# Kernel optimization log

Measured on AMD Instinct MI355X. Metric: run time of the kernel, lower is better.

The kernel has to match this reference:

```python
import jax, jax.numpy as jnp
import numpy as np

B, S, H = 2, 2048, 1024
N_HEADS = 16
HEAD_DIM = H // N_HEADS


def setup_inputs() -> dict:
    key = jax.random.key(0)
    ks = jax.random.split(key, 7)
    scale = 0.02
    return {
        "q": jax.random.normal(ks[0], (B, S, H), dtype=jnp.float32),
        "k": jax.random.normal(ks[1], (B, S, H), dtype=jnp.float32),
        "v": jax.random.normal(ks[2], (B, S, H), dtype=jnp.float32),
        "Wq": jax.random.normal(ks[3], (H, H), dtype=jnp.float32) * scale,
        "Wk": jax.random.normal(ks[4], (H, H), dtype=jnp.float32) * scale,
        "Wv": jax.random.normal(ks[5], (H, H), dtype=jnp.float32) * scale,
        "Wo": jax.random.normal(ks[6], (H, H), dtype=jnp.float32) * scale,
    }


def reference(q, k, v, Wq, Wk, Wv, Wo):
    b, i, _ = q.shape
    _, j, _ = k.shape
    # torch.nn.Linear(bias=False): y = x @ W.T
    qp = q @ Wq.T
    kp = k @ Wk.T
    vp = v @ Wv.T
    # NOTE: original uses .view(b, n_heads, i, head_dim) with NO transpose,
    # i.e. a raw reshape of the (b, i, hidden) layout. Replicate exactly.
    qh = qp.reshape(b, N_HEADS, i, HEAD_DIM)
    kh = kp.reshape(b, N_HEADS, j, HEAD_DIM)
    vh = vp.reshape(b, N_HEADS, j, HEAD_DIM)
    attn_score = jnp.einsum("bnid,bnjd->bnij", qh, kh) / (HEAD_DIM ** 0.5)
    attn_weight = jax.nn.softmax(attn_score, axis=3)
    x = jnp.einsum("bnij,bnjd->bnid", attn_weight, vh)  # [b, n, i, d]
    # rearrange 'b n i d -> b i (n d)'
    x = jnp.transpose(x, (0, 2, 1, 3)).reshape(b, i, H)
    out = x @ Wo.T
    return (out, attn_weight)
```

## Files before the change

### kernel.cpp

```cpp
#include <hip/hip_runtime.h>
#include <hip/hip_bf16.h>

#define DEVI __device__ __forceinline__

constexpr int kS  = 2048;
constexpr int kH  = 1024;
constexpr int kD  = 64;
constexpr int kBS = 4096;
constexpr int kHeadEls = kS * kD;

typedef __attribute__((ext_vector_type(4))) float f32x4;
typedef __attribute__((ext_vector_type(8))) __bf16 bf16x8;
typedef __attribute__((ext_vector_type(8))) unsigned short u16x8;
typedef __attribute__((ext_vector_type(2))) unsigned int u32x2;

DEVI unsigned short f2bf(float f) {
  unsigned int u = __builtin_bit_cast(unsigned int, f);
  u = u + 0x7FFFu + ((u >> 16) & 1u);
  return (unsigned short)(u >> 16);
}
DEVI float fast_exp2(float x) { float r; asm("v_exp_f32 %0, %1" : "=v"(r) : "v"(x)); return r; }
DEVI unsigned int cvt_pk(float lo, float hi) {
  unsigned int r; asm("v_cvt_pk_bf16_f32 %0, %1, %2" : "=v"(r) : "v"(lo), "v"(hi)); return r;
}
DEVI bf16x8 cvt8(const f32x4 a, const f32x4 b) {
  union { unsigned int u[4]; bf16x8 v; } r;
  r.u[0] = cvt_pk(a[0], a[1]); r.u[1] = cvt_pk(a[2], a[3]);
  r.u[2] = cvt_pk(b[0], b[1]); r.u[3] = cvt_pk(b[2], b[3]);
  return r.v;
}
DEVI float bf2f(unsigned int lo16) {
  return __builtin_bit_cast(float, lo16 << 16);
}

#define GLDS16(g, l) __builtin_amdgcn_global_load_lds( \
    (const __attribute__((address_space(1))) void*)(g), \
    (__attribute__((address_space(3))) void*)(l), 16, 0, 0)

__global__ __launch_bounds__(256) void cvt_w(
    const float* __restrict__ s0, const float* __restrict__ s1, const float* __restrict__ s2,
    unsigned short* __restrict__ d0, unsigned short* __restrict__ d1, unsigned short* __restrict__ d2)
{
  const int m = blockIdx.y;
  const float* s = m == 0 ? s0 : m == 1 ? s1 : s2;
  unsigned short* d = m == 0 ? d0 : m == 1 ? d1 : d2;
  const int i = (blockIdx.x * 256 + threadIdx.x) * 8;
  f32x4 a = *(const f32x4*)(s + i);
  f32x4 b = *(const f32x4*)(s + i + 4);
  union { unsigned int u[4]; u16x8 v; } r;
  r.u[0] = cvt_pk(a[0], a[1]); r.u[1] = cvt_pk(a[2], a[3]);
  r.u[2] = cvt_pk(b[0], b[1]); r.u[3] = cvt_pk(b[2], b[3]);
  *(u16x8*)(d + i) = r.v;
}

template<bool PROJ>
__global__ __launch_bounds__(256, 3) void gemm_k(
    const void* __restrict__ Aq, const void* __restrict__ Ak, const void* __restrict__ Av,
    const void* __restrict__ Bq, const void* __restrict__ Bk, const void* __restrict__ Bv,
    void* __restrict__ Cq, void* __restrict__ Ck, void* __restrict__ Cv)
{
  constexpr int K = kH;
  __shared__ __align__(16) unsigned char As[2][PROJ ? 16384 : 8192];
  __shared__ __align__(16) unsigned char Bs[2][PROJ ? 8192 : 16384];

  const int z = PROJ ? blockIdx.z : 0;
  const void* Ap = z == 0 ? Aq : z == 1 ? Ak : Av;
  const void* Bp = z == 0 ? Bq : z == 1 ? Bk : Bv;
  void*       Cp = z == 0 ? Cq : z == 1 ? Ck : Cv;

  const int tid  = threadIdx.x;
  const int lane = tid & 63, wv = tid >> 6;
  const int l15  = lane & 15, lg = lane >> 4;
  const int m0 = blockIdx.y * 128, n0 = blockIdx.x * 128;
  const int wM = (wv & 1) * 64, wN = (wv >> 1) * 64;

  const char* aSrc[PROJ ? 4 : 2];
  if constexpr (PROJ) {
#pragma unroll
    for (int c = 0; c < 4; ++c) {
      const int row = c * 32 + wv * 8 + (lane >> 3);
      const int cb  = ((lane & 7) * 16) ^ ((row & 7) << 4);
      aSrc[c] = (const char*)Ap + ((size_t)(m0 + row) * K) * 4 + cb;
    }
  } else {
#pragma unroll
    for (int c = 0; c < 2; ++c) {
      const int row = c * 64 + (tid >> 2);
      const int cb  = ((tid & 3) * 16) ^ (((row >> 1) & 3) << 4);
      aSrc[c] = (const char*)Ap + ((size_t)(m0 + row) * K) * 2 + cb;
    }
  }
  const char* bSrc[PROJ ? 2 : 4];
  if constexpr (PROJ) {
#pragma unroll
    for (int c = 0; c < 2; ++c) {
      const int row = c * 64 + (tid >> 2);
      const int cb  = ((tid & 3) * 16) ^ (((row >> 1) & 3) << 4);
      bSrc[c] = (const char*)Bp + ((size_t)(n0 + row) * K) * 2 + cb;
    }
  } else {
#pragma unroll
    for (int c = 0; c < 4; ++c) {
      const int row = c * 32 + wv * 8 + (lane >> 3);
      const int cb  = ((lane & 7) * 16) ^ ((row & 7) << 4);
      bSrc[c] = (const char*)Bp + ((size_t)(n0 + row) * K) * 4 + cb;
    }
  }

  int aoff[4], boff[4];
#pragma unroll
  for (int t = 0; t < 4; ++t) {
    const int rA = wM + t * 16 + l15;
    aoff[t] = PROJ ? (rA * 128 + ((lg * 32) ^ ((rA & 7) << 4)))
                   : (rA * 64  + ((lg * 16) ^ (((rA >> 1) & 3) << 4)));
    const int rB = wN + t * 16 + l15;
    boff[t] = PROJ ? (rB * 64  + ((lg * 16) ^ (((rB >> 1) & 3) << 4)))
                   : (rB * 128 + ((lg * 32) ^ ((rB & 7) << 4)));
  }

  f32x4 acc[4][4];
#pragma unroll
  for (int i = 0; i < 4; ++i)
#pragma unroll
    for (int j = 0; j < 4; ++j) acc[i][j] = {0.f, 0.f, 0.f, 0.f};

  auto STG = [&](int kk, int bb) {
    if constexpr (PROJ) {
#pragma unroll
      for (int c = 0; c < 4; ++c)
        GLDS16(aSrc[c] + (size_t)kk * 4, &As[bb][c * 4096 + wv * 1024]);
#pragma unroll
      for (int c = 0; c < 2; ++c)
        GLDS16(bSrc[c] + (size_t)kk * 2, &Bs[bb][c * 4096 + wv * 1024]);
    } else {
#pragma unroll
      for (int c = 0; c < 2; ++c)
        GLDS16(aSrc[c] + (size_t)kk * 2, &As[bb][c * 4096 + wv * 1024]);
#pragma unroll
      for (int c = 0; c < 4; ++c)
        GLDS16(bSrc[c] + (size_t)kk * 4, &Bs[bb][c * 4096 + wv * 1024]);
    }
  };

  STG(0, 0);
  __syncthreads();
  int cur = 0;
  for (int t = 0; t < K / 32; ++t) {
    if (t < K / 32 - 1) STG((t + 1) * 32, cur ^ 1);
    bf16x8 af[4], bfr[4];
#pragma unroll
    for (int x = 0; x < 4; ++x) {
      if constexpr (PROJ) {
        f32x4 p0 = *(const f32x4*)&As[cur][aoff[x]];
        f32x4 p1 = *(const f32x4*)&As[cur][aoff[x] ^ 16];
        af[x] = cvt8(p0, p1);
        bfr[x] = *(const bf16x8*)&Bs[cur][boff[x]];
      } else {
        af[x] = *(const bf16x8*)&As[cur][aoff[x]];
        f32x4 q0 = *(const f32x4*)&Bs[cur][boff[x]];
        f32x4 q1 = *(const f32x4*)&Bs[cur][boff[x] ^ 16];
        bfr[x] = cvt8(q0, q1);
      }
    }
#pragma unroll
    for (int mt = 0; mt < 4; ++mt)
#pragma unroll
      for (int nt = 0; nt < 4; ++nt)
        acc[mt][nt] = __builtin_amdgcn_mfma_f32_16x16x32_bf16(af[mt], bfr[nt], acc[mt][nt], 0, 0, 0);
    __syncthreads();
    cur ^= 1;
  }

  if constexpr (PROJ) {
    const bool vmode = (z == 2);
#pragma unroll
    for (int mt = 0; mt < 4; ++mt)
#pragma unroll
      for (int nt = 0; nt < 4; ++nt)
#pragma unroll
        for (int r = 0; r < 4; ++r) {
          const int row = m0 + wM + mt * 16 + lg * 4 + r;
          const int col = n0 + wN + nt * 16 + l15;
          const unsigned short hv = f2bf(acc[mt][nt][r]);
          if (!vmode) {
            ((unsigned short*)Cp)[(size_t)row * kH + col] = hv;
          } else {
            const int bn = row >> 7;
            const int j  = ((row & 127) << 4) | (col >> 6);
            const int d  = col & 63;
            ((unsigned short*)Cp)[(size_t)bn * kHeadEls + (size_t)d * kS + j] = hv;
          }
        }
  } else {
#pragma unroll
    for (int mt = 0; mt < 4; ++mt)
#pragma unroll
      for (int nt = 0; nt < 4; ++nt)
#pragma unroll
        for (int r = 0; r < 4; ++r) {
          const int row = m0 + wM + mt * 16 + lg * 4 + r;
          const int col = n0 + wN + nt * 16 + l15;
          __builtin_nontemporal_store(acc[mt][nt][r], (float*)Cp + (size_t)row * kH + col);
        }
  }
}

__global__ __launch_bounds__(128, 2) void attn_rs(
    const unsigned short* __restrict__ QP,
    const unsigned short* __restrict__ KP,
    float* __restrict__ rsout)
{
  __shared__ __align__(16) unsigned short Kb[2][4096];

  const int tid  = threadIdx.x;
  const int lane = tid & 63, wv = tid >> 6;
  const int l15  = lane & 15, lg = lane >> 4;
  const int f = blockIdx.x;
  const int x = f & 7, r8 = f >> 3;
  const int bn = (r8 >> 5) * 8 + x;
  const int i0 = (r8 & 31) * 64;

  const char* Khb = (const char*)(KP + (size_t)bn * kHeadEls);
  const unsigned short* Qh = QP + (size_t)bn * kHeadEls;

  const int srw = tid >> 3, scl = (tid & 7) * 16;
  const int kbase = srw * 128 + (scl ^ ((srw & 7) << 4));

  auto STAGE = [&](int j0, int bb) {
#pragma unroll
    for (int p = 0; p < 4; ++p)
      GLDS16(Khb + (size_t)j0 * 128 + kbase + p * 2048, (char*)Kb[bb] + p * 2048 + tid * 16);
  };

  int koff[4][2];
#pragma unroll
  for (int ct = 0; ct < 4; ++ct) {
    const int rK = ct * 16 + l15;
#pragma unroll
    for (int h = 0; h < 2; ++h)
      koff[ct][h] = rK * 128 + ((h * 64 + lg * 16) ^ ((rK & 7) << 4));
  }

  bf16x8 qf[2][2];
#pragma unroll
  for (int m = 0; m < 2; ++m) {
    const int qr = i0 + wv * 32 + m * 16 + l15;
#pragma unroll
    for (int h = 0; h < 2; ++h)
      qf[m][h] = *(const bf16x8*)(Qh + (size_t)qr * kD + h * 32 + lg * 8);
  }
  const float cexp = 0.18033688011112042f;

  float rs[2] = {0.f, 0.f};
  STAGE(0, 0);
  __syncthreads();
  int cur = 0;
  for (int t = 0; t < 32; ++t) {
    if (t < 31) STAGE((t + 1) * 64, cur ^ 1);
#pragma unroll
    for (int ct = 0; ct < 4; ++ct) {
      const bf16x8 kb0 = *(const bf16x8*)((const char*)Kb[cur] + koff[ct][0]);
      const bf16x8 kb1 = *(const bf16x8*)((const char*)Kb[cur] + koff[ct][1]);
#pragma unroll
      for (int m = 0; m < 2; ++m) {
        f32x4 s = {0.f, 0.f, 0.f, 0.f};
        s = __builtin_amdgcn_mfma_f32_16x16x32_bf16(kb0, qf[m][0], s, 0, 0, 0);
        s = __builtin_amdgcn_mfma_f32_16x16x32_bf16(kb1, qf[m][1], s, 0, 0, 0);
        const float w0 = fast_exp2(s[0] * cexp), w1 = fast_exp2(s[1] * cexp);
        const float w2 = fast_exp2(s[2] * cexp), w3 = fast_exp2(s[3] * cexp);
        rs[m] += (w0 + w1) + (w2 + w3);
      }
    }
    __syncthreads();
    cur ^= 1;
  }
#pragma unroll
  for (int m = 0; m < 2; ++m) {
    rs[m] += __shfl_xor(rs[m], 16, 64);
    rs[m] += __shfl_xor(rs[m], 32, 64);
  }
  if (lg == 0) {
#pragma unroll
    for (int m = 0; m < 2; ++m)
      rsout[(size_t)bn * kS + i0 + wv * 32 + m * 16 + l15] = rs[m];
  }
}

__global__ __launch_bounds__(128, 2) void attn_main(
    const unsigned short* __restrict__ QP,
    const unsigned short* __restrict__ KP,
    const unsigned short* __restrict__ VPT,
    const float* __restrict__ rsb,
    float* __restrict__ AW,
    unsigned short* __restrict__ XB)
{
  __shared__ __align__(16) unsigned short Kb[2][4096];
  __shared__ __align__(16) unsigned short Vb[2][4096];
  __shared__ __align__(16) unsigned short Ws[4096];

  const int tid  = threadIdx.x;
  const int lane = tid & 63, wv = tid >> 6;
  const int l15  = lane & 15, lg = lane >> 4;
  const int f = blockIdx.x;
  const int x = f & 7, r8 = f >> 3;
  const int bn = (r8 >> 5) * 8 + x;
  const int i0 = (r8 & 31) * 64;
  const int b = bn >> 4, n = bn & 15;

  const char* Khb = (const char*)(KP + (size_t)bn * kHeadEls);
  const char* Vhb = (const char*)(VPT + (size_t)bn * kHeadEls);
  const unsigned short* Qh = QP + (size_t)bn * kHeadEls;

  const int srw = tid >> 3, scl = (tid & 7) * 16;
  const int sswz = scl ^ ((srw & 7) << 4);
  const int kbase = srw * 128 + sswz;
  const int vbase = srw * 4096 + sswz;

  auto STAGE_KV = [&](int j0, int bb) {
#pragma unroll
    for (int p = 0; p < 4; ++p) {
      GLDS16(Khb + (size_t)j0 * 128 + kbase + p * 2048,
             (char*)Kb[bb] + p * 2048 + tid * 16);
      GLDS16(Vhb + (size_t)j0 * 2 + vbase + (size_t)p * 65536,
             (char*)Vb[bb] + p * 2048 + tid * 16);
    }
  };

  int koff[4][2], voff[2][4], wswr[2][4], wsrd[2][2];
#pragma unroll
  for (int ct = 0; ct < 4; ++ct) {
    const int rK = ct * 16 + l15;
#pragma unroll
    for (int h = 0; h < 2; ++h)
      koff[ct][h] = rK * 128 + ((h * 64 + lg * 16) ^ ((rK & 7) << 4));
  }
#pragma unroll
  for (int jc = 0; jc < 2; ++jc)
#pragma unroll
    for (int dt = 0; dt < 4; ++dt) {
      const int d = dt * 16 + l15;
      voff[jc][dt] = d * 128 + ((jc * 64 + lg * 16) ^ ((d & 7) << 4));
    }
#pragma unroll
  for (int m = 0; m < 2; ++m) {
    const int rw = wv * 32 + m * 16 + l15;
#pragma unroll
    for (int ct = 0; ct < 4; ++ct)
      wswr[m][ct] = rw * 128 + ((ct * 32 + lg * 8) ^ ((rw & 7) << 4));
#pragma unroll
    for (int jc = 0; jc < 2; ++jc)
      wsrd[m][jc] = rw * 128 + ((jc * 64 + lg * 16) ^ ((rw & 7) << 4));
  }

  int awrd[8];
  float* awp[8];
#pragma unroll
  for (int u = 0; u < 8; ++u) {
    const int rw = wv * 32 + u * 4 + lg;
    awrd[u] = rw * 128 + ((l15 * 8) ^ ((rw & 7) << 4));
    awp[u]  = AW + ((size_t)bn * kS + i0 + rw) * kS + l15 * 4;
  }

  bf16x8 qf[2][2];
  float inv[2];
#pragma unroll
  for (int m = 0; m < 2; ++m) {
    const int qr = i0 + wv * 32 + m * 16 + l15;
#pragma unroll
    for (int h = 0; h < 2; ++h)
      qf[m][h] = *(const bf16x8*)(Qh + (size_t)qr * kD + h * 32 + lg * 8);
    inv[m] = 1.0f / rsb[(size_t)bn * kS + qr];
  }
  const float cexp = 0.18033688011112042f;

  f32x4 pv[2][4];
#pragma unroll
  for (int m = 0; m < 2; ++m)
#pragma unroll
    for (int dt = 0; dt < 4; ++dt) pv[m][dt] = {0.f, 0.f, 0.f, 0.f};

  STAGE_KV(0, 0);
  asm volatile("s_waitcnt vmcnt(0) lgkmcnt(0)" ::: "memory");
  __builtin_amdgcn_sched_barrier(0);
  __builtin_amdgcn_s_barrier();

  int cur = 0;
  for (int t = 0; t < 32; ++t) {
    if (t < 31) STAGE_KV((t + 1) * 64, cur ^ 1);
    __builtin_amdgcn_sched_barrier(0);
#pragma unroll
    for (int ct = 0; ct < 4; ++ct) {
      const bf16x8 kb0 = *(const bf16x8*)((const char*)Kb[cur] + koff[ct][0]);
      const bf16x8 kb1 = *(const bf16x8*)((const char*)Kb[cur] + koff[ct][1]);
#pragma unroll
      for (int m = 0; m < 2; ++m) {
        f32x4 s = {0.f, 0.f, 0.f, 0.f};
        s = __builtin_amdgcn_mfma_f32_16x16x32_bf16(kb0, qf[m][0], s, 0, 0, 0);
        s = __builtin_amdgcn_mfma_f32_16x16x32_bf16(kb1, qf[m][1], s, 0, 0, 0);
        f32x4 w;
#pragma unroll
        for (int r = 0; r < 4; ++r) w[r] = fast_exp2(s[r] * cexp) * inv[m];
        u32x2 pk; pk[0] = cvt_pk(w[0], w[1]); pk[1] = cvt_pk(w[2], w[3]);
        *(u32x2*)((char*)Ws + wswr[m][ct]) = pk;
      }
    }
#pragma unroll
    for (int jc = 0; jc < 2; ++jc) {
      const bf16x8 pa0 = *(const bf16x8*)((const char*)Ws + wsrd[0][jc]);
      const bf16x8 pa1 = *(const bf16x8*)((const char*)Ws + wsrd[1][jc]);
#pragma unroll
      for (int dt = 0; dt < 4; ++dt) {
        const bf16x8 vf = *(const bf16x8*)((const char*)Vb[cur] + voff[jc][dt]);
        pv[0][dt] = __builtin_amdgcn_mfma_f32_16x16x32_bf16(pa0, vf, pv[0][dt], 0, 0, 0);
        pv[1][dt] = __builtin_amdgcn_mfma_f32_16x16x32_bf16(pa1, vf, pv[1][dt], 0, 0, 0);
      }
    }
#pragma unroll
    for (int u = 0; u < 8; ++u) {
      const u32x2 pk = *(const u32x2*)((const char*)Ws + awrd[u]);
      f32x4 w;
      w[0] = bf2f(pk[0] & 0xFFFFu);
      w[1] = bf2f(pk[0] >> 16);
      w[2] = bf2f(pk[1] & 0xFFFFu);
      w[3] = bf2f(pk[1] >> 16);
      __builtin_nontemporal_store(w, (f32x4*)(awp[u] + t * 64));
    }
    if (t < 31) {
      asm volatile("s_waitcnt vmcnt(8) lgkmcnt(0)" ::: "memory");
      __builtin_amdgcn_sched_barrier(0);
      __builtin_amdgcn_s_barrier();
    }
    cur ^= 1;
  }

#pragma unroll
  for (int m = 0; m < 2; ++m)
#pragma unroll
    for (int dt = 0; dt < 4; ++dt)
#pragma unroll
      for (int r = 0; r < 4; ++r) {
        const int row = b * kS + i0 + wv * 32 + m * 16 + lg * 4 + r;
        const int col = n * 64 + dt * 16 + l15;
        XB[(size_t)row * kH + col] = f2bf(pv[m][dt][r]);
      }
}

extern "C" void kernel_launch(void* const* d_in, const int* in_sizes, int n_in,
                              void* d_out, int out_size, void* d_ws, size_t ws_size,
                              hipStream_t stream) {
  const float* q  = (const float*)d_in[0];
  const float* k  = (const float*)d_in[1];
  const float* v  = (const float*)d_in[2];
  const float* Wq = (const float*)d_in[3];
  const float* Wk = (const float*)d_in[4];
  const float* Wv = (const float*)d_in[5];
  const float* Wo = (const float*)d_in[6];

  float* out = (float*)d_out;
  float* aw  = out + (size_t)kBS * kH;
  float* rsb = out;

  unsigned short* QP  = (unsigned short*)d_ws;
  unsigned short* KP  = QP  + (size_t)kBS * kH;
  unsigned short* VPT = KP  + (size_t)kBS * kH;
  unsigned short* XB  = VPT + (size_t)kBS * kH;

  unsigned short* stash = (unsigned short*)aw;
  unsigned short* Wqb = stash;
  unsigned short* Wkb = stash + (size_t)kH * kH;
  unsigned short* Wvb = stash + (size_t)2 * kH * kH;

  cvt_w<<<dim3(512, 3), 256, 0, stream>>>(Wq, Wk, Wv, Wqb, Wkb, Wvb);
  gemm_k<true><<<dim3(8, 32, 3), 256, 0, stream>>>(q, k, v, Wqb, Wkb, Wvb, QP, KP, VPT);
  attn_rs<<<dim3(1024), 128, 0, stream>>>(QP, KP, rsb);
  attn_main<<<dim3(1024), 128, 0, stream>>>(QP, KP, VPT, rsb, aw, XB);
  gemm_k<false><<<dim3(8, 32, 1), 256, 0, stream>>>(XB, XB, XB, Wo, Wo, Wo, out, out, out);
}
```

Before: 280.7 us.

## Double attention block rows to 128 and narrow output GEMM tile to 128x64

The attention kernels now run 256 threads (four waves) per block covering 128 query rows. Each staged K/V tile is therefore shared by twice as many rows, halving the block count and the redundant K/V loads. The output projection gets its own kernel with 128x64 tiles and 512 blocks, giving more parallelism for the single fp32-weight GEMM. The cost is more LDS per attention block (a larger Ws buffer) and changed occupancy bounds.

After: 261.1 us. 7.0% less time.

```diff
diff --git a/kernel.cpp b/kernel.cpp
--- a/kernel.cpp
+++ b/kernel.cpp
@@ -53,17 +53,16 @@
   *(u16x8*)(d + i) = r.v;
 }
 
-template<bool PROJ>
-__global__ __launch_bounds__(256, 3) void gemm_k(
+__global__ __launch_bounds__(256, 3) void gemm_p(
     const void* __restrict__ Aq, const void* __restrict__ Ak, const void* __restrict__ Av,
     const void* __restrict__ Bq, const void* __restrict__ Bk, const void* __restrict__ Bv,
     void* __restrict__ Cq, void* __restrict__ Ck, void* __restrict__ Cv)
 {
   constexpr int K = kH;
-  __shared__ __align__(16) unsigned char As[2][PROJ ? 16384 : 8192];
-  __shared__ __align__(16) unsigned char Bs[2][PROJ ? 8192 : 16384];
-
-  const int z = PROJ ? blockIdx.z : 0;
+  __shared__ __align__(16) unsigned char As[2][16384];
+  __shared__ __align__(16) unsigned char Bs[2][8192];
+
+  const int z = blockIdx.z;
   const void* Ap = z == 0 ? Aq : z == 1 ? Ak : Av;
   const void* Bp = z == 0 ? Bq : z == 1 ? Bk : Bv;
   void*       Cp = z == 0 ? Cq : z == 1 ? Ck : Cv;
@@ -74,48 +73,28 @@
   const int m0 = blockIdx.y * 128, n0 = blockIdx.x * 128;
   const int wM = (wv & 1) * 64, wN = (wv >> 1) * 64;
 
-  const char* aSrc[PROJ ? 4 : 2];
-  if constexpr (PROJ) {
-#pragma unroll
-    for (int c = 0; c < 4; ++c) {
-      const int row = c * 32 + wv * 8 + (lane >> 3);
-      const int cb  = ((lane & 7) * 16) ^ ((row & 7) << 4);
-      aSrc[c] = (const char*)Ap + ((size_t)(m0 + row) * K) * 4 + cb;
-    }
-  } else {
-#pragma unroll
-    for (int c = 0; c < 2; ++c) {
-      const int row = c * 64 + (tid >> 2);
-      const int cb  = ((tid & 3) * 16) ^ (((row >> 1) & 3) << 4);
-      aSrc[c] = (const char*)Ap + ((size_t)(m0 + row) * K) * 2 + cb;
-    }
-  }
-  const char* bSrc[PROJ ? 2 : 4];
-  if constexpr (PROJ) {
-#pragma unroll
-    for (int c = 0; c < 2; ++c) {
-      const int row = c * 64 + (tid >> 2);
-      const int cb  = ((tid & 3) * 16) ^ (((row >> 1) & 3) << 4);
-      bSrc[c] = (const char*)Bp + ((size_t)(n0 + row) * K) * 2 + cb;
-    }
-  } else {
-#pragma unroll
-    for (int c = 0; c < 4; ++c) {
-      const int row = c * 32 + wv * 8 + (lane >> 3);
-      const int cb  = ((lane & 7) * 16) ^ ((row & 7) << 4);
-      bSrc[c] = (const char*)Bp + ((size_t)(n0 + row) * K) * 4 + cb;
-    }
+  const char* aSrc[4];
+#pragma unroll
+  for (int c = 0; c < 4; ++c) {
+    const int row = c * 32 + wv * 8 + (lane >> 3);
+    const int cb  = ((lane & 7) * 16) ^ ((row & 7) << 4);
+    aSrc[c] = (const char*)Ap + ((size_t)(m0 + row) * K) * 4 + cb;
+  }
+  const char* bSrc[2];
+#pragma unroll
+  for (int c = 0; c < 2; ++c) {
+    const int row = c * 64 + (tid >> 2);
+    const int cb  = ((tid & 3) * 16) ^ (((row >> 1) & 3) << 4);
+    bSrc[c] = (const char*)Bp + ((size_t)(n0 + row) * K) * 2 + cb;
   }
 
   int aoff[4], boff[4];
 #pragma unroll
   for (int t = 0; t < 4; ++t) {
     const int rA = wM + t * 16 + l15;
-    aoff[t] = PROJ ? (rA * 128 + ((lg * 32) ^ ((rA & 7) << 4)))
-                   : (rA * 64  + ((lg * 16) ^ (((rA >> 1) & 3) << 4)));
+    aoff[t] = rA * 128 + ((lg * 32) ^ ((rA & 7) << 4));
     const int rB = wN + t * 16 + l15;
-    boff[t] = PROJ ? (rB * 64  + ((lg * 16) ^ (((rB >> 1) & 3) << 4)))
-                   : (rB * 128 + ((lg * 32) ^ ((rB & 7) << 4)));
+    boff[t] = rB * 64 + ((lg * 16) ^ (((rB >> 1) & 3) << 4));
   }
 
   f32x4 acc[4][4];
@@ -125,21 +104,12 @@
     for (int j = 0; j < 4; ++j) acc[i][j] = {0.f, 0.f, 0.f, 0.f};
 
   auto STG = [&](int kk, int bb) {
-    if constexpr (PROJ) {
-#pragma unroll
-      for (int c = 0; c < 4; ++c)
-        GLDS16(aSrc[c] + (size_t)kk * 4, &As[bb][c * 4096 + wv * 1024]);
-#pragma unroll
-      for (int c = 0; c < 2; ++c)
-        GLDS16(bSrc[c] + (size_t)kk * 2, &Bs[bb][c * 4096 + wv * 1024]);
-    } else {
-#pragma unroll
-      for (int c = 0; c < 2; ++c)
-        GLDS16(aSrc[c] + (size_t)kk * 2, &As[bb][c * 4096 + wv * 1024]);
-#pragma unroll
-      for (int c = 0; c < 4; ++c)
-        GLDS16(bSrc[c] + (size_t)kk * 4, &Bs[bb][c * 4096 + wv * 1024]);
-    }
+#pragma unroll
+    for (int c = 0; c < 4; ++c)
+      GLDS16(aSrc[c] + (size_t)kk * 4, &As[bb][c * 4096 + wv * 1024]);
+#pragma unroll
+    for (int c = 0; c < 2; ++c)
+      GLDS16(bSrc[c] + (size_t)kk * 2, &Bs[bb][c * 4096 + wv * 1024]);
   };
 
   STG(0, 0);
@@ -150,17 +120,10 @@
     bf16x8 af[4], bfr[4];
 #pragma unroll
     for (int x = 0; x < 4; ++x) {
-      if constexpr (PROJ) {
-        f32x4 p0 = *(const f32x4*)&As[cur][aoff[x]];
-        f32x4 p1 = *(const f32x4*)&As[cur][aoff[x] ^ 16];
-        af[x] = cvt8(p0, p1);
-        bfr[x] = *(const bf16x8*)&Bs[cur][boff[x]];
-      } else {
-        af[x] = *(const bf16x8*)&As[cur][aoff[x]];
-        f32x4 q0 = *(const f32x4*)&Bs[cur][boff[x]];
-        f32x4 q1 = *(const f32x4*)&Bs[cur][boff[x] ^ 16];
-        bfr[x] = cvt8(q0, q1);
-      }
+      f32x4 p0 = *(const f32x4*)&As[cur][aoff[x]];
+      f32x4 p1 = *(const f32x4*)&As[cur][aoff[x] ^ 16];
+      af[x] = cvt8(p0, p1);
+      bfr[x] = *(const bf16x8*)&Bs[cur][boff[x]];
     }
 #pragma unroll
     for (int mt = 0; mt < 4; ++mt)
@@ -171,41 +134,119 @@
     cur ^= 1;
   }
 
-  if constexpr (PROJ) {
-    const bool vmode = (z == 2);
+  const bool vmode = (z == 2);
+#pragma unroll
+  for (int mt = 0; mt < 4; ++mt)
+#pragma unroll
+    for (int nt = 0; nt < 4; ++nt)
+#pragma unroll
+      for (int r = 0; r < 4; ++r) {
+        const int row = m0 + wM + mt * 16 + lg * 4 + r;
+        const int col = n0 + wN + nt * 16 + l15;
+        const unsigned short hv = f2bf(acc[mt][nt][r]);
+        if (!vmode) {
+          ((unsigned short*)Cp)[(size_t)row * kH + col] = hv;
+        } else {
+          const int bn = row >> 7;
+          const int j  = ((row & 127) << 4) | (col >> 6);
+          const int d  = col & 63;
+          ((unsigned short*)Cp)[(size_t)bn * kHeadEls + (size_t)d * kS + j] = hv;
+        }
+      }
+}
+
+__global__ __launch_bounds__(256, 3) void gemm_f(
+    const unsigned short* __restrict__ Ap, const float* __restrict__ Bp,
+    float* __restrict__ Cp)
+{
+  constexpr int K = kH;
+  __shared__ __align__(16) unsigned char As[2][8192];
+  __shared__ __align__(16) unsigned char Bs[2][8192];
+
+  const int tid  = threadIdx.x;
+  const int lane = tid & 63, wv = tid >> 6;
+  const int l15  = lane & 15, lg = lane >> 4;
+  const int m0 = blockIdx.y * 128, n0 = blockIdx.x * 64;
+  const int wM = (wv & 1) * 64, wN = (wv >> 1) * 32;
+
+  const char* aSrc[2];
+#pragma unroll
+  for (int c = 0; c < 2; ++c) {
+    const int row = c * 64 + (tid >> 2);
+    const int cb  = ((tid & 3) * 16) ^ (((row >> 1) & 3) << 4);
+    aSrc[c] = (const char*)Ap + ((size_t)(m0 + row) * K) * 2 + cb;
+  }
+  const char* bSrc[2];
+#pragma unroll
+  for (int c = 0; c < 2; ++c) {
+    const int row = c * 32 + (tid >> 3);
+    const int cb  = ((tid & 7) * 16) ^ ((row & 7) << 4);
+    bSrc[c] = (const char*)Bp + ((size_t)(n0 + row) * K) * 4 + cb;
+  }
+
+  int aoff[4], boff[2];
+#pragma unroll
+  for (int t = 0; t < 4; ++t) {
+    const int rA = wM + t * 16 + l15;
+    aoff[t] = rA * 64 + ((lg * 16) ^ (((rA >> 1) & 3) << 4));
+  }
+#pragma unroll
+  for (int t = 0; t < 2; ++t) {
+    const int rB = wN + t * 16 + l15;
+    boff[t] = rB * 128 + ((lg * 32) ^ ((rB & 7) << 4));
+  }
+
+  f32x4 acc[4][2];
+#pragma unroll
+  for (int i = 0; i < 4; ++i)
+#pragma unroll
+    for (int j = 0; j < 2; ++j) acc[i][j] = {0.f, 0.f, 0.f, 0.f};
+
+  auto STG = [&](int kk, int bb) {
+#pragma unroll
+    for (int c = 0; c < 2; ++c) {
+      GLDS16(aSrc[c] + (size_t)kk * 2, &As[bb][c * 4096 + wv * 1024]);
+      GLDS16(bSrc[c] + (size_t)kk * 4, &Bs[bb][c * 4096 + wv * 1024]);
+    }
+  };
+
+  STG(0, 0);
+  __syncthreads();
+  int cur = 0;
+  for (int t = 0; t < K / 32; ++t) {
+    if (t < K / 32 - 1) STG((t + 1) * 32, cur ^ 1);
+    bf16x8 af[4], bfr[2];
+#pragma unroll
+    for (int x = 0; x < 4; ++x)
+      af[x] = *(const bf16x8*)&As[cur][aoff[x]];
+#pragma unroll
+    for (int x = 0; x < 2; ++x) {
+      f32x4 q0 = *(const f32x4*)&Bs[cur][boff[x]];
+      f32x4 q1 = *(const f32x4*)&Bs[cur][boff[x] ^ 16];
+      bfr[x] = cvt8(q0, q1);
+    }
 #pragma unroll
     for (int mt = 0; mt < 4; ++mt)
 #pragma unroll
-      for (int nt = 0; nt < 4; ++nt)
-#pragma unroll
-        for (int r = 0; r < 4; ++r) {
-          const int row = m0 + wM + mt * 16 + lg * 4 + r;
-          const int col = n0 + wN + nt * 16 + l15;
-          const unsigned short hv = f2bf(acc[mt][nt][r]);
-          if (!vmode) {
-            ((unsigned short*)Cp)[(size_t)row * kH + col] = hv;
-          } else {
-            const int bn = row >> 7;
-            const int j  = ((row & 127) << 4) | (col >> 6);
-            const int d  = col & 63;
-            ((unsigned short*)Cp)[(size_t)bn * kHeadEls + (size_t)d * kS + j] = hv;
-          }
-        }
-  } else {
-#pragma unroll
-    for (int mt = 0; mt < 4; ++mt)
-#pragma unroll
-      for (int nt = 0; nt < 4; ++nt)
-#pragma unroll
-        for (int r = 0; r < 4; ++r) {
-          const int row = m0 + wM + mt * 16 + lg * 4 + r;
-          const int col = n0 + wN + nt * 16 + l15;
-          __builtin_nontemporal_store(acc[mt][nt][r], (float*)Cp + (size_t)row * kH + col);
-        }
-  }
-}
-
-__global__ __launch_bounds__(128, 2) void attn_rs(
+      for (int nt = 0; nt < 2; ++nt)
+        acc[mt][nt] = __builtin_amdgcn_mfma_f32_16x16x32_bf16(af[mt], bfr[nt], acc[mt][nt], 0, 0, 0);
+    __syncthreads();
+    cur ^= 1;
+  }
+
+#pragma unroll
+  for (int mt = 0; mt < 4; ++mt)
+#pragma unroll
+    for (int nt = 0; nt < 2; ++nt)
+#pragma unroll
+      for (int r = 0; r < 4; ++r) {
+        const int row = m0 + wM + mt * 16 + lg * 4 + r;
+        const int col = n0 + wN + nt * 16 + l15;
+        __builtin_nontemporal_store(acc[mt][nt][r], Cp + (size_t)row * kH + col);
+      }
+}
+
+__global__ __launch_bounds__(256, 2) void attn_rs(
     const unsigned short* __restrict__ QP,
     const unsigned short* __restrict__ KP,
     float* __restrict__ rsout)
@@ -216,20 +257,23 @@
   const int lane = tid & 63, wv = tid >> 6;
   const int l15  = lane & 15, lg = lane >> 4;
   const int f = blockIdx.x;
-  const int x = f & 7, r8 = f >> 3;
-  const int bn = (r8 >> 5) * 8 + x;
-  const int i0 = (r8 & 31) * 64;
+  const int x = f & 7, r = f >> 3;
+  const int bn = (r >> 4) * 8 + x;
+  const int i0 = (r & 15) * 128;
 
   const char* Khb = (const char*)(KP + (size_t)bn * kHeadEls);
   const unsigned short* Qh = QP + (size_t)bn * kHeadEls;
 
-  const int srw = tid >> 3, scl = (tid & 7) * 16;
-  const int kbase = srw * 128 + (scl ^ ((srw & 7) << 4));
-
+  int kbase[2];
+#pragma unroll
+  for (int p = 0; p < 2; ++p) {
+    const int row = p * 32 + (tid >> 3);
+    kbase[p] = row * 128 + (((tid & 7) * 16) ^ ((row & 7) << 4));
+  }
   auto STAGE = [&](int j0, int bb) {
 #pragma unroll
-    for (int p = 0; p < 4; ++p)
-      GLDS16(Khb + (size_t)j0 * 128 + kbase + p * 2048, (char*)Kb[bb] + p * 2048 + tid * 16);
+    for (int p = 0; p < 2; ++p)
+      GLDS16(Khb + (size_t)j0 * 128 + kbase[p], (char*)Kb[bb] + p * 4096 + tid * 16);
   };
 
   int koff[4][2];
@@ -286,7 +330,7 @@
   }
 }
 
-__global__ __launch_bounds__(128, 2) void attn_main(
+__global__ __launch_bounds__(256, 3) void attn_main(
     const unsigned short* __restrict__ QP,
     const unsigned short* __restrict__ KP,
     const unsigned short* __restrict__ VPT,
@@ -296,33 +340,34 @@
 {
   __shared__ __align__(16) unsigned short Kb[2][4096];
   __shared__ __align__(16) unsigned short Vb[2][4096];
-  __shared__ __align__(16) unsigned short Ws[4096];
+  __shared__ __align__(16) unsigned short Ws[8192];
 
   const int tid  = threadIdx.x;
   const int lane = tid & 63, wv = tid >> 6;
   const int l15  = lane & 15, lg = lane >> 4;
   const int f = blockIdx.x;
-  const int x = f & 7, r8 = f >> 3;
-  const int bn = (r8 >> 5) * 8 + x;
-  const int i0 = (r8 & 31) * 64;
+  const int x = f & 7, r = f >> 3;
+  const int bn = (r >> 4) * 8 + x;
+  const int i0 = (r & 15) * 128;
   const int b = bn >> 4, n = bn & 15;
 
   const char* Khb = (const char*)(KP + (size_t)bn * kHeadEls);
   const char* Vhb = (const char*)(VPT + (size_t)bn * kHeadEls);
   const unsigned short* Qh = QP + (size_t)bn * kHeadEls;
 
-  const int srw = tid >> 3, scl = (tid & 7) * 16;
-  const int sswz = scl ^ ((srw & 7) << 4);
-  const int kbase = srw * 128 + sswz;
-  const int vbase = srw * 4096 + sswz;
-
+  int kbase[2], vbase[2];
+#pragma unroll
+  for (int p = 0; p < 2; ++p) {
+    const int row = p * 32 + (tid >> 3);
+    const int sw  = ((tid & 7) * 16) ^ ((row & 7) << 4);
+    kbase[p] = row * 128 + sw;
+    vbase[p] = row * 4096 + sw;
+  }
   auto STAGE_KV = [&](int j0, int bb) {
 #pragma unroll
-    for (int p = 0; p < 4; ++p) {
-      GLDS16(Khb + (size_t)j0 * 128 + kbase + p * 2048,
-             (char*)Kb[bb] + p * 2048 + tid * 16);
-      GLDS16(Vhb + (size_t)j0 * 2 + vbase + (size_t)p * 65536,
-             (char*)Vb[bb] + p * 2048 + tid * 16);
+    for (int p = 0; p < 2; ++p) {
+      GLDS16(Khb + (size_t)j0 * 128 + kbase[p], (char*)Kb[bb] + p * 4096 + tid * 16);
+      GLDS16(Vhb + (size_t)j0 * 2 + vbase[p],   (char*)Vb[bb] + p * 4096 + tid * 16);
     }
   };
 
@@ -399,7 +444,7 @@
         s = __builtin_amdgcn_mfma_f32_16x16x32_bf16(kb1, qf[m][1], s, 0, 0, 0);
         f32x4 w;
 #pragma unroll
-        for (int r = 0; r < 4; ++r) w[r] = fast_exp2(s[r] * cexp) * inv[m];
+        for (int r2 = 0; r2 < 4; ++r2) w[r2] = fast_exp2(s[r2] * cexp) * inv[m];
         u32x2 pk; pk[0] = cvt_pk(w[0], w[1]); pk[1] = cvt_pk(w[2], w[3]);
         *(u32x2*)((char*)Ws + wswr[m][ct]) = pk;
       }
@@ -438,10 +483,10 @@
 #pragma unroll
     for (int dt = 0; dt < 4; ++dt)
 #pragma unroll
-      for (int r = 0; r < 4; ++r) {
-        const int row = b * kS + i0 + wv * 32 + m * 16 + lg * 4 + r;
+      for (int r2 = 0; r2 < 4; ++r2) {
+        const int row = b * kS + i0 + wv * 32 + m * 16 + lg * 4 + r2;
         const int col = n * 64 + dt * 16 + l15;
-        XB[(size_t)row * kH + col] = f2bf(pv[m][dt][r]);
+        XB[(size_t)row * kH + col] = f2bf(pv[m][dt][r2]);
       }
 }
 
@@ -471,8 +516,8 @@
   unsigned short* Wvb = stash + (size_t)2 * kH * kH;
 
   cvt_w<<<dim3(512, 3), 256, 0, stream>>>(Wq, Wk, Wv, Wqb, Wkb, Wvb);
-  gemm_k<true><<<dim3(8, 32, 3), 256, 0, stream>>>(q, k, v, Wqb, Wkb, Wvb, QP, KP, VPT);
-  attn_rs<<<dim3(1024), 128, 0, stream>>>(QP, KP, rsb);
-  attn_main<<<dim3(1024), 128, 0, stream>>>(QP, KP, VPT, rsb, aw, XB);
-  gemm_k<false><<<dim3(8, 32, 1), 256, 0, stream>>>(XB, XB, XB, Wo, Wo, Wo, out, out, out);
-}
+  gemm_p<<<dim3(8, 32, 3), 256, 0, stream>>>(q, k, v, Wqb, Wkb, Wvb, QP, KP, VPT);
+  attn_rs<<<dim3(512), 256, 0, stream>>>(QP, KP, rsb);
+  attn_main<<<dim3(512), 256, 0, stream>>>(QP, KP, VPT, rsb, aw, XB);
+  gemm_f<<<dim3(16, 32), 256, 0, stream>>>(XB, Wo, out);
+}
```
